# Optimization experiments

Hardware: AMD Instinct MI355X
Metric: run time of the kernel (lower is better)

The kernel has to match this reference:

```python
import jax, jax.numpy as jnp
import numpy as np

B, N, L = 16, 512, 512          # batch, compound atoms, protein words
DIM = 10                         # compound feature dim
DM, H, DK, DFF = 128, 8, 16, 512 # transformer dims
LG, LO = 3, 3                    # layer_gnn, layer_output
NFP, NW = 10000, 10000           # vocab sizes
NEG = -9e15                      # GAT mask sentinel (matches torch code)


def _layernorm(x, g, b, eps=1e-6):
    # annotated-transformer LayerNorm: unbiased std, eps added to std
    m = jnp.mean(x, -1, keepdims=True)
    s = jnp.std(x, -1, keepdims=True, ddof=1)
    return g * (x - m) / (s + eps) + b


def _pos_encoding(length, d_model):
    pos = np.arange(length)[:, None]
    div = np.exp(np.arange(0, d_model, 2) * (-np.log(10000.0) / d_model))
    pe = np.zeros((length, d_model), np.float32)
    pe[:, 0::2] = np.sin(pos * div)
    pe[:, 1::2] = np.cos(pos * div)
    return jnp.asarray(pe)


def setup_inputs():
    ks = iter(jax.random.split(jax.random.key(0), 64))
    def nrm(shape, scale):
        return jax.random.normal(next(ks), shape, jnp.float32) * scale
    return dict(
        fingerprints=jax.random.randint(next(ks), (B, N), 0, NFP, jnp.int32),
        fp_mask=jnp.ones((B, N), jnp.float32),
        adjacency=jax.random.randint(next(ks), (B, N, N), 0, 2, jnp.int32),
        words=jax.random.randint(next(ks), (B, L), 0, NW, jnp.int32),
        words_mask=jnp.ones((B, L), jnp.float32),
        emb_fp=nrm((NFP, DIM), 0.1),
        emb_word=nrm((NW, DM), 0.1),
        Wg=nrm((LG, DIM, DIM), 0.3), bg=jnp.zeros((LG, DIM), jnp.float32),
        attn_a=nrm((LG, 2 * DIM), 0.3),
        Wq=nrm((DM, DM), 0.09), bq=jnp.zeros((DM,), jnp.float32),
        Wk=nrm((DM, DM), 0.09), bk=jnp.zeros((DM,), jnp.float32),
        Wv=nrm((DM, DM), 0.09), bv=jnp.zeros((DM,), jnp.float32),
        Wo=nrm((DM, DM), 0.09), bo=jnp.zeros((DM,), jnp.float32),
        ln1_g=jnp.ones((DM,), jnp.float32), ln1_b=jnp.zeros((DM,), jnp.float32),
        ln2_g=jnp.ones((DM,), jnp.float32), ln2_b=jnp.zeros((DM,), jnp.float32),
        lnf_g=jnp.ones((DM,), jnp.float32), lnf_b=jnp.zeros((DM,), jnp.float32),
        W1=nrm((DM, DFF), 0.09), b1=jnp.zeros((DFF,), jnp.float32),
        W2=nrm((DFF, DM), 0.045), b2=jnp.zeros((DM,), jnp.float32),
        Wtout=nrm((DM, DIM), 0.09), btout=jnp.zeros((DIM,), jnp.float32),
        Watt=nrm((DIM, DIM), 0.3), batt=jnp.zeros((DIM,), jnp.float32),
        Wout=nrm((LO, 2 * DIM, 2 * DIM), 0.2), bout=jnp.zeros((LO, 2 * DIM), jnp.float32),
        Wint=nrm((2 * DIM, 2), 0.2), bint=jnp.zeros((2,), jnp.float32),
    )


def _forward(fingerprints, fp_mask, adjacency, words, words_mask,
             emb_fp, emb_word, Wg, bg, attn_a,
             Wq, bq, Wk, bk, Wv, bv, Wo, bo,
             ln1_g, ln1_b, ln2_g, ln2_b, lnf_g, lnf_b,
             W1, b1, W2, b2, Wtout, btout,
             Watt, batt, Wout, bout, Wint, bint):
    # ---- GAT over compound graph (dropout disabled = eval/deterministic) ----
    xs = emb_fp[fingerprints]                     # [B,N,DIM]
    mask = fp_mask[:, :, None]                    # [B,N,1]
    adj = adjacency > 0
    for i in range(LG):
        h = jax.nn.relu(xs @ Wg[i] + bg[i]) * mask
        # e[b,i,j] = leaky_relu(a1.h_i + a2.h_j)  == leaky_relu([h_i||h_j] @ a)
        s1 = h @ attn_a[i, :DIM]                  # [B,N]
        s2 = h @ attn_a[i, DIM:]                  # [B,N]
        e = jax.nn.leaky_relu(s1[:, :, None] + s2[:, None, :])  # [B,N,N]
        att = jax.nn.softmax(jnp.where(adj, e, NEG), axis=2)
        xs = xs + att @ h
    compound = jnp.mean(xs * mask, axis=1, keepdims=True)       # [B,1,DIM]

    # ---- transformer encoder, 1 layer, annotated-transformer (pre-norm) ----
    x = emb_word[words] * jnp.sqrt(jnp.float32(DM)) + _pos_encoding(L, DM)
    m4 = words_mask[:, None, None, :] > 0         # [B,1,1,L]
    xn = _layernorm(x, ln1_g, ln1_b)
    heads = lambda t: t.reshape(B, L, H, DK).transpose(0, 2, 1, 3)
    q, k, v = heads(xn @ Wq + bq), heads(xn @ Wk + bk), heads(xn @ Wv + bv)
    scores = jnp.einsum('bhqd,bhkd->bhqk', q, k) / jnp.sqrt(jnp.float32(DK))
    p = jax.nn.softmax(jnp.where(m4, scores, -1e9), axis=-1)
    attn = jnp.einsum('bhqk,bhkd->bhqd', p, v).transpose(0, 2, 1, 3).reshape(B, L, DM)
    x = x + (attn @ Wo + bo)
    xn = _layernorm(x, ln2_g, ln2_b)
    x = x + (jax.nn.relu(xn @ W1 + b1) @ W2 + b2)
    x = _layernorm(x, lnf_g, lnf_b)
    word_vectors = jax.nn.relu(x) @ Wtout + btout  # [B,L,DIM]

    # ---- tanh cross-attention (attention_cnn) ----
    hc = jax.nn.relu(compound @ Watt + batt)       # [B,1,DIM]
    hp = jax.nn.relu(word_vectors @ Watt + batt)   # [B,L,DIM]
    w = jnp.tanh(jnp.einsum('bxd,bld->bxl', hc, hp))  # [B,1,L]
    protein = jnp.mean(w.transpose(0, 2, 1) * hp, axis=1, keepdims=True)  # [B,1,DIM]

    cat = jnp.concatenate([compound, protein], axis=2)  # [B,1,2*DIM]
    for j in range(LO):
        cat = jax.nn.relu(cat @ Wout[j] + bout[j])
    return jnp.squeeze(cat @ Wint + bint, axis=1)        # [B,2]


def reference(fingerprints, fp_mask, adjacency, words, words_mask,
              emb_fp, emb_word, Wg, bg, attn_a,
              Wq, bq, Wk, bk, Wv, bv, Wo, bo,
              ln1_g, ln1_b, ln2_g, ln2_b, lnf_g, lnf_b,
              W1, b1, W2, b2, Wtout, btout,
              Watt, batt, Wout, bout, Wint, bint):
    return _forward(fingerprints, fp_mask, adjacency, words, words_mask,
                    emb_fp, emb_word, Wg, bg, attn_a,
                    Wq, bq, Wk, bk, Wv, bv, Wo, bo,
                    ln1_g, ln1_b, ln2_g, ln2_b, lnf_g, lnf_b,
                    W1, b1, W2, b2, Wtout, btout,
                    Watt, batt, Wout, bout, Wint, bint)
```

## Files before the change

kernel.cpp:

```cpp
#include <hip/hip_runtime.h>
#include <hip/hip_bf16.h>
#include <math.h>

#define B 16
#define N 512
#define L 512
#define DIM 10
#define DM 128
#define H 8
#define DK 16
#define DFF 512
#define LG 3
#define LO 3
#define NEGV -9.0e15f
#define RF 16
#define AQR 64

__device__ __forceinline__ float wave_reduce_sum(float v) {
    #pragma unroll
    for (int o = 32; o > 0; o >>= 1) v += __shfl_down(v, o, 64);
    return v;
}

__device__ __forceinline__ float quad_sum(float x) {
    int y1 = __builtin_amdgcn_mov_dpp(__float_as_int(x), 0xB1, 0xF, 0xF, true);
    float s = x + __int_as_float(y1);
    int y2 = __builtin_amdgcn_mov_dpp(__float_as_int(s), 0x4E, 0xF, 0xF, true);
    return s + __int_as_float(y2);
}


__global__ void k_embed_fp(const int* __restrict__ fing, const float* __restrict__ emb_fp,
                           float* __restrict__ xs) {
    int idx = blockIdx.x * blockDim.x + threadIdx.x;
    if (idx >= B * N * DIM) return;
    int d = idx % DIM;
    int bn = idx / DIM;
    xs[idx] = emb_fp[fing[bn] * DIM + d];
}

__global__ void k_gnn_h(const float* __restrict__ xs, const float* __restrict__ fp_mask,
                        const float* __restrict__ Wg, const float* __restrict__ bg,
                        const float* __restrict__ aatt,
                        float* __restrict__ h, float* __restrict__ s1, float* __restrict__ s2) {
    int bn = blockIdx.x * blockDim.x + threadIdx.x;
    if (bn >= B * N) return;
    float x[DIM];
    #pragma unroll
    for (int d = 0; d < DIM; d++) x[d] = xs[bn * DIM + d];
    float m = fp_mask[bn];
    float a1 = 0.f, a2 = 0.f;
    #pragma unroll
    for (int j = 0; j < DIM; j++) {
        float acc = bg[j];
        #pragma unroll
        for (int d = 0; d < DIM; d++) acc += x[d] * Wg[d * DIM + j];
        acc = fmaxf(acc, 0.f) * m;
        h[bn * DIM + j] = acc;
        a1 += acc * aatt[j];
        a2 += acc * aatt[DIM + j];
    }
    s1[bn] = a1;
    s2[bn] = a2;
}

__global__ void k_gnn_att(const float* __restrict__ h, const float* __restrict__ s1,
                          const float* __restrict__ s2, const int* __restrict__ adj,
                          float* __restrict__ xs) {
    int b  = blockIdx.x / (N / 16);
    int rg = blockIdx.x % (N / 16);
    int t = threadIdx.x;
    int g  = t >> 4;
    int ll = t & 15;
    int i = rg * 16 + g;

    __shared__ float h_s[N * DIM];
    __shared__ float s2_s[N];

    const float* hb = h + (long)b * N * DIM;
    for (int idx = t; idx < N * DIM; idx += 256) h_s[idx] = hb[idx];
    for (int j = t; j < N; j += 256) s2_s[j] = s2[b * N + j];
    __syncthreads();

    float s1v = s1[b * N + i];
    const int* adjrow = adj + ((long)b * N + i) * N;

    float e[32];
    #pragma unroll
    for (int c = 0; c < 32; c++) {
        int j = c * 16 + ll;
        float xsc = s1v + s2_s[j];
        xsc = xsc > 0.f ? xsc : 0.01f * xsc;
        e[c] = (adjrow[j] > 0) ? xsc : NEGV;
    }
    float m = e[0];
    #pragma unroll
    for (int c = 1; c < 32; c++) m = fmaxf(m, e[c]);
    #pragma unroll
    for (int off = 1; off < 16; off <<= 1) m = fmaxf(m, __shfl_xor(m, off, 64));

    float sum = 0.f;
    float a[DIM];
    #pragma unroll
    for (int d = 0; d < DIM; d++) a[d] = 0.f;
    #pragma unroll
    for (int c = 0; c < 32; c++) {
        float p = expf(e[c] - m);
        sum += p;
        int j = c * 16 + ll;
        #pragma unroll
        for (int d = 0; d < DIM; d++) a[d] += p * h_s[j * DIM + d];
    }
    #pragma unroll
    for (int off = 1; off < 16; off <<= 1) {
        sum += __shfl_xor(sum, off, 64);
        #pragma unroll
        for (int d = 0; d < DIM; d++) a[d] += __shfl_xor(a[d], off, 64);
    }
    if (ll < DIM) {
        float av = a[0];
        if (ll == 1) av = a[1]; else if (ll == 2) av = a[2]; else if (ll == 3) av = a[3];
        else if (ll == 4) av = a[4]; else if (ll == 5) av = a[5]; else if (ll == 6) av = a[6];
        else if (ll == 7) av = a[7]; else if (ll == 8) av = a[8]; else if (ll == 9) av = a[9];
        xs[((long)b * N + i) * DIM + ll] += av / sum;
    }
}

__global__ void k_compound(const float* __restrict__ xs, const float* __restrict__ fp_mask,
                           const float* __restrict__ Watt, const float* __restrict__ batt,
                           float* __restrict__ compound, float* __restrict__ hc) {
    int b = blockIdx.x;
    int t = threadIdx.x;
    int wid = t >> 6, lane = t & 63;
    float lacc[DIM];
    #pragma unroll
    for (int d = 0; d < DIM; d++) lacc[d] = 0.f;
    for (int n = t; n < N; n += 256) {
        float m = fp_mask[b * N + n];
        #pragma unroll
        for (int d = 0; d < DIM; d++) lacc[d] += xs[((long)b * N + n) * DIM + d] * m;
    }
    __shared__ float red[4][DIM];
    __shared__ float comp_s[DIM];
    #pragma unroll
    for (int d = 0; d < DIM; d++) lacc[d] = wave_reduce_sum(lacc[d]);
    if (lane == 0) {
        #pragma unroll
        for (int d = 0; d < DIM; d++) red[wid][d] = lacc[d];
    }
    __syncthreads();
    if (t < DIM) {
        float c = (red[0][t] + red[1][t] + red[2][t] + red[3][t]) / (float)N;
        compound[b * DIM + t] = c;
        comp_s[t] = c;
    }
    __syncthreads();
    if (t < DIM) {
        float acc = batt[t];
        #pragma unroll
        for (int e = 0; e < DIM; e++) acc += comp_s[e] * Watt[e * DIM + t];
        hc[b * DIM + t] = fmaxf(acc, 0.f);
    }
}


__global__ void k_pe(float* __restrict__ pe) {
    int idx = blockIdx.x * blockDim.x + threadIdx.x;
    if (idx >= L * DM) return;
    int d = idx % DM, l = idx / DM;
    int k = d >> 1;
    double div = exp((double)(2 * k) * (-log(10000.0) / (double)DM));
    double ang = (double)l * div;
    pe[idx] = (d & 1) ? (float)cos(ang) : (float)sin(ang);
}

__global__ void k_embed_word(const int* __restrict__ words, const float* __restrict__ emb,
                             const float* __restrict__ pe, float* __restrict__ x) {
    long idx = (long)blockIdx.x * blockDim.x + threadIdx.x;
    if (idx >= (long)B * L * DM) return;
    int d = idx % DM;
    long bl = idx / DM;
    int l = (int)(bl % L);
    x[idx] = emb[(long)words[bl] * DM + d] * sqrtf(128.0f) + pe[l * DM + d];
}

__global__ void k_layernorm(const float* __restrict__ x, const float* __restrict__ g,
                            const float* __restrict__ bb, float* __restrict__ out) {
    int row = blockIdx.x;
    int t = threadIdx.x;
    int wid = t >> 6, lane = t & 63;
    float v = x[(long)row * DM + t];
    float s = wave_reduce_sum(v);
    __shared__ float r2[2], r3[2];
    if (lane == 0) r2[wid] = s;
    __syncthreads();
    float mean = (r2[0] + r2[1]) / (float)DM;
    float dv = v - mean;
    float q = wave_reduce_sum(dv * dv);
    if (lane == 0) r3[wid] = q;
    __syncthreads();
    float sd = sqrtf((r3[0] + r3[1]) / (float)(DM - 1)) + 1e-6f;
    out[(long)row * DM + t] = g[t] * dv / sd + bb[t];
}

__global__ void k_qkv(const float* __restrict__ xn,
                      const float* __restrict__ Wq, const float* __restrict__ bq,
                      const float* __restrict__ Wk, const float* __restrict__ bk,
                      const float* __restrict__ Wv, const float* __restrict__ bv,
                      float* __restrict__ q, float* __restrict__ k, float* __restrict__ v) {
    long row0 = (long)blockIdx.x * RF;
    int t = threadIdx.x;
    __shared__ float xs_s[RF * DM];
    for (int i = t; i < RF * DM; i += 384) xs_s[i] = xn[row0 * DM + i];
    __syncthreads();
    int proj = t / DM;
    int j = t % DM;
    const float* W    = proj == 0 ? Wq : (proj == 1 ? Wk : Wv);
    const float* bias = proj == 0 ? bq : (proj == 1 ? bk : bv);
    float* out        = proj == 0 ? q  : (proj == 1 ? k  : v);
    float acc[RF];
    #pragma unroll
    for (int r = 0; r < RF; r++) acc[r] = bias[j];
    for (int d = 0; d < DM; d++) {
        float w = W[d * DM + j];
        #pragma unroll
        for (int r = 0; r < RF; r++) acc[r] += xs_s[r * DM + d] * w;
    }
    #pragma unroll
    for (int r = 0; r < RF; r++) {
        long row = row0 + r;
        int b = (int)(row / L), l = (int)(row % L);
        out[(((long)b * H + j / DK) * L + l) * DK + (j % DK)] = acc[r];
    }
}

__global__ void __launch_bounds__(256, 4)
k_attn(const float* __restrict__ q, const float* __restrict__ k,
       const float* __restrict__ v, const float* __restrict__ wmask,
       float* __restrict__ attnout) {
    int blk = blockIdx.x;
    int qc = blk % (L / AQR);
    int bh = blk / (L / AQR);
    int b = bh / H, hh = bh % H;
    int t = threadIdx.x;
    int sl = t & 3;
    int r = t >> 2;
    int l = qc * AQR + r;

    __shared__ float4 k_s[L * 4];
    __shared__ float wm_s[L];
    const float4* kb4 = (const float4*)(k + (long)bh * L * DK);
    for (int i = t; i < L * 4; i += 256) k_s[i] = kb4[i];
    for (int j = t; j < L; j += 256) wm_s[j] = (wmask[b * L + j] > 0.f) ? 0.f : -1e9f;
    __syncthreads();

    float4 qr = ((const float4*)(q + ((long)bh * L + l) * DK))[sl];
    qr.x *= 0.25f; qr.y *= 0.25f; qr.z *= 0.25f; qr.w *= 0.25f;

    const float4* vb4 = (const float4*)(v + (long)bh * L * DK);

    float m = -1e30f, ssum = 0.f;
    float4 acc = make_float4(0.f, 0.f, 0.f, 0.f);

    for (int c = 0; c < L / 8; c++) {
        int j0 = c * 8;
        float s8[8];
        #pragma unroll
        for (int jj = 0; jj < 8; jj++) {
            float4 kk = k_s[(j0 + jj) * 4 + sl];
            float part = qr.x * kk.x + qr.y * kk.y + qr.z * kk.z + qr.w * kk.w;
            s8[jj] = quad_sum(part);
        }
        const float4* mp = (const float4*)&wm_s[j0];
        float4 ma = mp[0], mb = mp[1];
        s8[0] += ma.x; s8[1] += ma.y; s8[2] += ma.z; s8[3] += ma.w;
        s8[4] += mb.x; s8[5] += mb.y; s8[6] += mb.z; s8[7] += mb.w;

        float cm = fmaxf(fmaxf(fmaxf(s8[0], s8[1]), fmaxf(s8[2], s8[3])),
                         fmaxf(fmaxf(s8[4], s8[5]), fmaxf(s8[6], s8[7])));
        float mn = fmaxf(m, cm);
        float scale = __expf(m - mn);
        ssum *= scale;
        acc.x *= scale; acc.y *= scale; acc.z *= scale; acc.w *= scale;
        m = mn;
        #pragma unroll
        for (int jj = 0; jj < 8; jj++) {
            float p = __expf(s8[jj] - m);
            ssum += p;
            float4 vv = vb4[(j0 + jj) * 4 + sl];
            acc.x += p * vv.x; acc.y += p * vv.y; acc.z += p * vv.z; acc.w += p * vv.w;
        }
    }

    float inv = 1.f / ssum;
    float4* outp = (float4*)(attnout + ((long)b * L + l) * DM + hh * DK);
    outp[sl] = make_float4(acc.x * inv, acc.y * inv, acc.z * inv, acc.w * inv);
}

__global__ void k_oproj(const float* __restrict__ attnout, const float* __restrict__ Wo,
                        const float* __restrict__ bo, float* __restrict__ x) {
    long row0 = (long)blockIdx.x * RF;
    int t = threadIdx.x;
    __shared__ float a_s[RF * DM];
    for (int i = t; i < RF * DM; i += 128) a_s[i] = attnout[row0 * DM + i];
    __syncthreads();
    float acc[RF];
    #pragma unroll
    for (int r = 0; r < RF; r++) acc[r] = bo[t];
    for (int d = 0; d < DM; d++) {
        float w = Wo[d * DM + t];
        #pragma unroll
        for (int r = 0; r < RF; r++) acc[r] += a_s[r * DM + d] * w;
    }
    #pragma unroll
    for (int r = 0; r < RF; r++) x[(row0 + r) * DM + t] += acc[r];
}

__global__ void k_ffn(const float* __restrict__ xn, const float* __restrict__ W1,
                      const float* __restrict__ b1, const float* __restrict__ W2,
                      const float* __restrict__ b2, float* __restrict__ x) {
    long row0 = (long)blockIdx.x * RF;
    int t = threadIdx.x;
    __shared__ float xs_s[RF * DM];
    __shared__ float h_s[RF * DFF];
    for (int i = t; i < RF * DM; i += 512) xs_s[i] = xn[row0 * DM + i];
    __syncthreads();
    {
        float acc[RF];
        #pragma unroll
        for (int r = 0; r < RF; r++) acc[r] = b1[t];
        for (int d = 0; d < DM; d++) {
            float w = W1[d * DFF + t];
            #pragma unroll
            for (int r = 0; r < RF; r++) acc[r] += xs_s[r * DM + d] * w;
        }
        #pragma unroll
        for (int r = 0; r < RF; r++) h_s[r * DFF + t] = fmaxf(acc[r], 0.f);
    }
    __syncthreads();
    int col = t & 127, rq = t >> 7;
    float acc2[4];
    #pragma unroll
    for (int rr = 0; rr < 4; rr++) acc2[rr] = b2[col];
    for (int f = 0; f < DFF; f++) {
        float w = W2[f * DM + col];
        #pragma unroll
        for (int rr = 0; rr < 4; rr++) acc2[rr] += h_s[(rq * 4 + rr) * DFF + f] * w;
    }
    #pragma unroll
    for (int rr = 0; rr < 4; rr++) x[(row0 + rq * 4 + rr) * DM + col] += acc2[rr];
}

__global__ void k_lnf_hp(const float* __restrict__ x, const float* __restrict__ g,
                         const float* __restrict__ bb, const float* __restrict__ Wtout,
                         const float* __restrict__ btout, const float* __restrict__ Watt,
                         const float* __restrict__ batt, float* __restrict__ hp) {
    int row = blockIdx.x;
    int t = threadIdx.x;
    int wid = t >> 6, lane = t & 63;
    float v = x[(long)row * DM + t];
    float s = wave_reduce_sum(v);
    __shared__ float r2[2], r3[2];
    if (lane == 0) r2[wid] = s;
    __syncthreads();
    float mean = (r2[0] + r2[1]) / (float)DM;
    float dv = v - mean;
    float qq = wave_reduce_sum(dv * dv);
    if (lane == 0) r3[wid] = qq;
    __syncthreads();
    float sd = sqrtf((r3[0] + r3[1]) / (float)(DM - 1)) + 1e-6f;
    float xnv = g[t] * dv / sd + bb[t];
    __shared__ float rrelu[DM];
    rrelu[t] = fmaxf(xnv, 0.f);
    __syncthreads();
    __shared__ float wv_s[DIM];
    if (t < DIM) {
        float acc = btout[t];
        for (int d = 0; d < DM; d++) acc += rrelu[d] * Wtout[d * DIM + t];
        wv_s[t] = acc;
    }
    __syncthreads();
    if (t < DIM) {
        float acc = batt[t];
        #pragma unroll
        for (int e = 0; e < DIM; e++) acc += wv_s[e] * Watt[e * DIM + t];
        hp[(long)row * DIM + t] = fmaxf(acc, 0.f);
    }
}

__global__ void k_final(const float* __restrict__ hp, const float* __restrict__ hc,
                        const float* __restrict__ compound, const float* __restrict__ Wout,
                        const float* __restrict__ bout, const float* __restrict__ Wint,
                        const float* __restrict__ bint, float* __restrict__ out) {
    int b = blockIdx.x;
    int t = threadIdx.x;
    int wid = t >> 6, lane = t & 63;

    __shared__ float wout_s[LO * 2 * DIM * 2 * DIM];
    __shared__ float bout_s[LO * 2 * DIM];
    __shared__ float wint_s[2 * DIM * 2];
    __shared__ float bint_s[2];
    __shared__ float hc_s[DIM];
    __shared__ float red[4][DIM];
    __shared__ float cat_s[2 * DIM];
    __shared__ float tmp_s[2 * DIM];

    for (int i = t; i < LO * 2 * DIM * 2 * DIM; i += 256) wout_s[i] = Wout[i];
    for (int i = t; i < LO * 2 * DIM; i += 256) bout_s[i] = bout[i];
    for (int i = t; i < 2 * DIM * 2; i += 256) wint_s[i] = Wint[i];
    if (t < 2) bint_s[t] = bint[t];
    if (t < DIM) hc_s[t] = hc[b * DIM + t];
    __syncthreads();

    float lacc[DIM];
    #pragma unroll
    for (int e = 0; e < DIM; e++) lacc[e] = 0.f;
    for (int l = t; l < L; l += 256) {
        const float* hpl = hp + ((long)b * L + l) * DIM;
        float hv[DIM];
        float dot = 0.f;
        #pragma unroll
        for (int e = 0; e < DIM; e++) { hv[e] = hpl[e]; dot += hc_s[e] * hv[e]; }
        float w = tanhf(dot);
        #pragma unroll
        for (int e = 0; e < DIM; e++) lacc[e] += w * hv[e];
    }
    #pragma unroll
    for (int e = 0; e < DIM; e++) lacc[e] = wave_reduce_sum(lacc[e]);
    if (lane == 0) {
        #pragma unroll
        for (int e = 0; e < DIM; e++) red[wid][e] = lacc[e];
    }
    __syncthreads();
    if (t < DIM) {
        cat_s[t] = compound[b * DIM + t];
        cat_s[DIM + t] = (red[0][t] + red[1][t] + red[2][t] + red[3][t]) / (float)L;
    }
    __syncthreads();

    for (int j = 0; j < LO; j++) {
        float acc = 0.f;
        if (t < 2 * DIM) {
            acc = bout_s[j * 2 * DIM + t];
            #pragma unroll
            for (int e = 0; e < 2 * DIM; e++)
                acc += cat_s[e] * wout_s[j * 2 * DIM * 2 * DIM + e * 2 * DIM + t];
            acc = fmaxf(acc, 0.f);
            tmp_s[t] = acc;
        }
        __syncthreads();
        if (t < 2 * DIM) cat_s[t] = tmp_s[t];
        __syncthreads();
    }
    if (t < 2) {
        float o = bint_s[t];
        #pragma unroll
        for (int e = 0; e < 2 * DIM; e++) o += cat_s[e] * wint_s[e * 2 + t];
        out[b * 2 + t] = o;
    }
}

extern "C" void kernel_launch(void* const* d_in, const int* in_sizes, int n_in,
                              void* d_out, int out_size, void* d_ws, size_t ws_size,
                              hipStream_t stream) {
    (void)in_sizes; (void)n_in; (void)out_size; (void)ws_size;
    const int*   fingerprints = (const int*)d_in[0];
    const float* fp_mask      = (const float*)d_in[1];
    const int*   adjacency    = (const int*)d_in[2];
    const int*   words        = (const int*)d_in[3];
    const float* words_mask   = (const float*)d_in[4];
    const float* emb_fp       = (const float*)d_in[5];
    const float* emb_word     = (const float*)d_in[6];
    const float* Wg   = (const float*)d_in[7];
    const float* bg   = (const float*)d_in[8];
    const float* attn_a = (const float*)d_in[9];
    const float* Wq = (const float*)d_in[10];
    const float* bq = (const float*)d_in[11];
    const float* Wk = (const float*)d_in[12];
    const float* bk = (const float*)d_in[13];
    const float* Wv = (const float*)d_in[14];
    const float* bv = (const float*)d_in[15];
    const float* Wo = (const float*)d_in[16];
    const float* bo = (const float*)d_in[17];
    const float* ln1_g = (const float*)d_in[18];
    const float* ln1_b = (const float*)d_in[19];
    const float* ln2_g = (const float*)d_in[20];
    const float* ln2_b = (const float*)d_in[21];
    const float* lnf_g = (const float*)d_in[22];
    const float* lnf_b = (const float*)d_in[23];
    const float* W1 = (const float*)d_in[24];
    const float* b1 = (const float*)d_in[25];
    const float* W2 = (const float*)d_in[26];
    const float* b2 = (const float*)d_in[27];
    const float* Wtout = (const float*)d_in[28];
    const float* btout = (const float*)d_in[29];
    const float* Watt  = (const float*)d_in[30];
    const float* batt  = (const float*)d_in[31];
    const float* Wout  = (const float*)d_in[32];
    const float* bout  = (const float*)d_in[33];
    const float* Wint  = (const float*)d_in[34];
    const float* bint  = (const float*)d_in[35];
    float* out = (float*)d_out;

    float* w = (float*)d_ws;
    float* xs = w;        w += B * N * DIM;
    float* h  = w;        w += B * N * DIM;
    float* s1 = w;        w += B * N;
    float* s2 = w;        w += B * N;
    float* compound = w;  w += B * DIM;
    float* hc = w;        w += B * DIM;
    float* pe = w;        w += L * DM;
    float* x  = w;        w += (long)B * L * DM;
    float* xn = w;        w += (long)B * L * DM;
    float* qb = w;        w += (long)B * H * L * DK;
    float* kb = w;        w += (long)B * H * L * DK;
    float* vb = w;        w += (long)B * H * L * DK;
    float* attnout = w;   w += (long)B * L * DM;
    float* hp = w;        w += (long)B * L * DIM;

    k_embed_fp<<<(B * N * DIM + 255) / 256, 256, 0, stream>>>(fingerprints, emb_fp, xs);
    for (int i = 0; i < LG; i++) {
        k_gnn_h<<<(B * N + 255) / 256, 256, 0, stream>>>(
            xs, fp_mask, Wg + i * DIM * DIM, bg + i * DIM, attn_a + i * 2 * DIM, h, s1, s2);
        k_gnn_att<<<B * (N / 16), 256, 0, stream>>>(h, s1, s2, adjacency, xs);
    }
    k_compound<<<B, 256, 0, stream>>>(xs, fp_mask, Watt, batt, compound, hc);

    k_pe<<<(L * DM + 255) / 256, 256, 0, stream>>>(pe);
    k_embed_word<<<(B * L * DM + 255) / 256, 256, 0, stream>>>(words, emb_word, pe, x);
    k_layernorm<<<B * L, DM, 0, stream>>>(x, ln1_g, ln1_b, xn);
    k_qkv<<<B * L / RF, 3 * DM, 0, stream>>>(xn, Wq, bq, Wk, bk, Wv, bv, qb, kb, vb);
    k_attn<<<B * H * (L / AQR), 256, 0, stream>>>(qb, kb, vb, words_mask, attnout);
    k_oproj<<<B * L / RF, DM, 0, stream>>>(attnout, Wo, bo, x);
    k_layernorm<<<B * L, DM, 0, stream>>>(x, ln2_g, ln2_b, xn);
    k_ffn<<<B * L / RF, DFF, 0, stream>>>(xn, W1, b1, W2, b2, x);
    k_lnf_hp<<<B * L, DM, 0, stream>>>(x, lnf_g, lnf_b, Wtout, btout, Watt, batt, hp);
    k_final<<<B, 256, 0, stream>>>(hp, hc, compound, Wout, bout, Wint, bint, out);
}
```

Before: 255.2 us.

## Fuse embedding with LayerNorm and LN2, FFN, final LN and head into one kernel

Merges word embedding and the first LayerNorm into one kernel. It also folds the second LayerNorm, the FFN, the final LayerNorm and the small output projections into a single per-16-row kernel, so the residual stream no longer round-trips through global memory between these stages. The QKV, O-projection and FFN matmul inner loops are unrolled by four with float4 shared-memory reads to cut LDS instruction count. The fused FFN kernel uses more shared memory per block (about 50KB), which may lower occupancy.

```diff
diff --git a/kernel.cpp b/kernel.cpp
--- a/kernel.cpp
+++ b/kernel.cpp
@@ -29,6 +29,12 @@
     return s + __int_as_float(y2);
 }
 
+__device__ __forceinline__ float half_reduce_sum(float v) {
+    #pragma unroll
+    for (int o = 16; o > 0; o >>= 1) v += __shfl_xor(v, o, 64);
+    return v;
+}
+
 
 __global__ void k_embed_fp(const int* __restrict__ fing, const float* __restrict__ emb_fp,
                            float* __restrict__ xs) {
@@ -174,22 +180,16 @@
     pe[idx] = (d & 1) ? (float)cos(ang) : (float)sin(ang);
 }
 
-__global__ void k_embed_word(const int* __restrict__ words, const float* __restrict__ emb,
-                             const float* __restrict__ pe, float* __restrict__ x) {
-    long idx = (long)blockIdx.x * blockDim.x + threadIdx.x;
-    if (idx >= (long)B * L * DM) return;
-    int d = idx % DM;
-    long bl = idx / DM;
-    int l = (int)(bl % L);
-    x[idx] = emb[(long)words[bl] * DM + d] * sqrtf(128.0f) + pe[l * DM + d];
-}
-
-__global__ void k_layernorm(const float* __restrict__ x, const float* __restrict__ g,
-                            const float* __restrict__ bb, float* __restrict__ out) {
+__global__ void k_embed_ln(const int* __restrict__ words, const float* __restrict__ emb,
+                           const float* __restrict__ pe, const float* __restrict__ g,
+                           const float* __restrict__ bb,
+                           float* __restrict__ x, float* __restrict__ xn) {
     int row = blockIdx.x;
     int t = threadIdx.x;
     int wid = t >> 6, lane = t & 63;
-    float v = x[(long)row * DM + t];
+    int l = row % L;
+    float v = emb[(long)words[row] * DM + t] * sqrtf(128.0f) + pe[l * DM + t];
+    x[(long)row * DM + t] = v;
     float s = wave_reduce_sum(v);
     __shared__ float r2[2], r3[2];
     if (lane == 0) r2[wid] = s;
@@ -200,7 +200,7 @@
     if (lane == 0) r3[wid] = q;
     __syncthreads();
     float sd = sqrtf((r3[0] + r3[1]) / (float)(DM - 1)) + 1e-6f;
-    out[(long)row * DM + t] = g[t] * dv / sd + bb[t];
+    xn[(long)row * DM + t] = g[t] * dv / sd + bb[t];
 }
 
 __global__ void k_qkv(const float* __restrict__ xn,
@@ -221,10 +221,16 @@
     float acc[RF];
     #pragma unroll
     for (int r = 0; r < RF; r++) acc[r] = bias[j];
-    for (int d = 0; d < DM; d++) {
-        float w = W[d * DM + j];
-        #pragma unroll
-        for (int r = 0; r < RF; r++) acc[r] += xs_s[r * DM + d] * w;
+    for (int d4 = 0; d4 < DM / 4; d4++) {
+        float w0 = W[(4 * d4 + 0) * DM + j];
+        float w1 = W[(4 * d4 + 1) * DM + j];
+        float w2 = W[(4 * d4 + 2) * DM + j];
+        float w3 = W[(4 * d4 + 3) * DM + j];
+        #pragma unroll
+        for (int r = 0; r < RF; r++) {
+            float4 xv = ((const float4*)&xs_s[r * DM])[d4];
+            acc[r] += xv.x * w0 + xv.y * w1 + xv.z * w2 + xv.w * w3;
+        }
     }
     #pragma unroll
     for (int r = 0; r < RF; r++) {
@@ -307,84 +313,142 @@
     float acc[RF];
     #pragma unroll
     for (int r = 0; r < RF; r++) acc[r] = bo[t];
-    for (int d = 0; d < DM; d++) {
-        float w = Wo[d * DM + t];
-        #pragma unroll
-        for (int r = 0; r < RF; r++) acc[r] += a_s[r * DM + d] * w;
+    for (int d4 = 0; d4 < DM / 4; d4++) {
+        float w0 = Wo[(4 * d4 + 0) * DM + t];
+        float w1 = Wo[(4 * d4 + 1) * DM + t];
+        float w2 = Wo[(4 * d4 + 2) * DM + t];
+        float w3 = Wo[(4 * d4 + 3) * DM + t];
+        #pragma unroll
+        for (int r = 0; r < RF; r++) {
+            float4 av = ((const float4*)&a_s[r * DM])[d4];
+            acc[r] += av.x * w0 + av.y * w1 + av.z * w2 + av.w * w3;
+        }
     }
     #pragma unroll
     for (int r = 0; r < RF; r++) x[(row0 + r) * DM + t] += acc[r];
 }
 
-__global__ void k_ffn(const float* __restrict__ xn, const float* __restrict__ W1,
-                      const float* __restrict__ b1, const float* __restrict__ W2,
-                      const float* __restrict__ b2, float* __restrict__ x) {
+__global__ void k_ffn_fused(const float* __restrict__ x,
+                            const float* __restrict__ ln2_g, const float* __restrict__ ln2_b,
+                            const float* __restrict__ W1, const float* __restrict__ b1,
+                            const float* __restrict__ W2, const float* __restrict__ b2,
+                            const float* __restrict__ lnf_g, const float* __restrict__ lnf_b,
+                            const float* __restrict__ Wtout, const float* __restrict__ btout,
+                            const float* __restrict__ Watt, const float* __restrict__ batt,
+                            float* __restrict__ hp) {
     long row0 = (long)blockIdx.x * RF;
     int t = threadIdx.x;
-    __shared__ float xs_s[RF * DM];
-    __shared__ float h_s[RF * DFF];
-    for (int i = t; i < RF * DM; i += 512) xs_s[i] = xn[row0 * DM + i];
-    __syncthreads();
+
+    __shared__ float x_s[RF][DM];
+    __shared__ float xn_s[RF][DM];
+    __shared__ float h_s[RF][DFF];
+    __shared__ float r_s[RF][DM + 4];
+    __shared__ float wt_s[DM * DIM];
+    __shared__ float wa_s[DIM * DIM];
+    __shared__ float bt_s[DIM], ba_s[DIM];
+    __shared__ float wv_s[RF][DIM];
+
+    {
+        float4 xv = ((const float4*)(x + row0 * DM))[t];
+        ((float4*)&x_s[0][0])[t] = xv;
+        for (int i = t; i < DM * DIM; i += 512) wt_s[i] = Wtout[i];
+        for (int i = t; i < DIM * DIM; i += 512) wa_s[i] = Watt[i];
+        if (t < DIM) { bt_s[t] = btout[t]; ba_s[t] = batt[t]; }
+    }
+    __syncthreads();
+
+    {
+        int row = t >> 5, c = t & 31;
+        float4 v = ((const float4*)&x_s[row][0])[c];
+        float s = half_reduce_sum(v.x + v.y + v.z + v.w);
+        float mean = s / (float)DM;
+        float4 dv = make_float4(v.x - mean, v.y - mean, v.z - mean, v.w - mean);
+        float q = half_reduce_sum(dv.x * dv.x + dv.y * dv.y + dv.z * dv.z + dv.w * dv.w);
+        float sd = sqrtf(q / (float)(DM - 1)) + 1e-6f;
+        const float4 g4 = ((const float4*)ln2_g)[c];
+        const float4 b4 = ((const float4*)ln2_b)[c];
+        ((float4*)&xn_s[row][0])[c] = make_float4(
+            g4.x * dv.x / sd + b4.x, g4.y * dv.y / sd + b4.y,
+            g4.z * dv.z / sd + b4.z, g4.w * dv.w / sd + b4.w);
+    }
+    __syncthreads();
+
     {
         float acc[RF];
         #pragma unroll
         for (int r = 0; r < RF; r++) acc[r] = b1[t];
-        for (int d = 0; d < DM; d++) {
-            float w = W1[d * DFF + t];
+        for (int d4 = 0; d4 < DM / 4; d4++) {
+            float w0 = W1[(4 * d4 + 0) * DFF + t];
+            float w1 = W1[(4 * d4 + 1) * DFF + t];
+            float w2 = W1[(4 * d4 + 2) * DFF + t];
+            float w3 = W1[(4 * d4 + 3) * DFF + t];
             #pragma unroll
-            for (int r = 0; r < RF; r++) acc[r] += xs_s[r * DM + d] * w;
-        }
-        #pragma unroll
-        for (int r = 0; r < RF; r++) h_s[r * DFF + t] = fmaxf(acc[r], 0.f);
-    }
-    __syncthreads();
-    int col = t & 127, rq = t >> 7;
-    float acc2[4];
-    #pragma unroll
-    for (int rr = 0; rr < 4; rr++) acc2[rr] = b2[col];
-    for (int f = 0; f < DFF; f++) {
-        float w = W2[f * DM + col];
-        #pragma unroll
-        for (int rr = 0; rr < 4; rr++) acc2[rr] += h_s[(rq * 4 + rr) * DFF + f] * w;
-    }
-    #pragma unroll
-    for (int rr = 0; rr < 4; rr++) x[(row0 + rq * 4 + rr) * DM + col] += acc2[rr];
-}
-
-__global__ void k_lnf_hp(const float* __restrict__ x, const float* __restrict__ g,
-                         const float* __restrict__ bb, const float* __restrict__ Wtout,
-                         const float* __restrict__ btout, const float* __restrict__ Watt,
-                         const float* __restrict__ batt, float* __restrict__ hp) {
-    int row = blockIdx.x;
-    int t = threadIdx.x;
-    int wid = t >> 6, lane = t & 63;
-    float v = x[(long)row * DM + t];
-    float s = wave_reduce_sum(v);
-    __shared__ float r2[2], r3[2];
-    if (lane == 0) r2[wid] = s;
-    __syncthreads();
-    float mean = (r2[0] + r2[1]) / (float)DM;
-    float dv = v - mean;
-    float qq = wave_reduce_sum(dv * dv);
-    if (lane == 0) r3[wid] = qq;
-    __syncthreads();
-    float sd = sqrtf((r3[0] + r3[1]) / (float)(DM - 1)) + 1e-6f;
-    float xnv = g[t] * dv / sd + bb[t];
-    __shared__ float rrelu[DM];
-    rrelu[t] = fmaxf(xnv, 0.f);
-    __syncthreads();
-    __shared__ float wv_s[DIM];
-    if (t < DIM) {
-        float acc = btout[t];
-        for (int d = 0; d < DM; d++) acc += rrelu[d] * Wtout[d * DIM + t];
-        wv_s[t] = acc;
-    }
-    __syncthreads();
-    if (t < DIM) {
-        float acc = batt[t];
-        #pragma unroll
-        for (int e = 0; e < DIM; e++) acc += wv_s[e] * Watt[e * DIM + t];
-        hp[(long)row * DIM + t] = fmaxf(acc, 0.f);
+            for (int r = 0; r < RF; r++) {
+                float4 xv = ((const float4*)&xn_s[r][0])[d4];
+                acc[r] += xv.x * w0 + xv.y * w1 + xv.z * w2 + xv.w * w3;
+            }
+        }
+        #pragma unroll
+        for (int r = 0; r < RF; r++) h_s[r][t] = fmaxf(acc[r], 0.f);
+    }
+    __syncthreads();
+
+    {
+        int col = t & 127, rq = t >> 7;
+        float acc2[4];
+        #pragma unroll
+        for (int rr = 0; rr < 4; rr++) acc2[rr] = b2[col];
+        for (int f4 = 0; f4 < DFF / 4; f4++) {
+            float w0 = W2[(4 * f4 + 0) * DM + col];
+            float w1 = W2[(4 * f4 + 1) * DM + col];
+            float w2 = W2[(4 * f4 + 2) * DM + col];
+            float w3 = W2[(4 * f4 + 3) * DM + col];
+            #pragma unroll
+            for (int rr = 0; rr < 4; rr++) {
+                float4 hv = ((const float4*)&h_s[rq * 4 + rr][0])[f4];
+                acc2[rr] += hv.x * w0 + hv.y * w1 + hv.z * w2 + hv.w * w3;
+            }
+        }
+        __syncthreads();
+        #pragma unroll
+        for (int rr = 0; rr < 4; rr++) {
+            int row = rq * 4 + rr;
+            xn_s[row][col] = x_s[row][col] + acc2[rr];
+        }
+    }
+    __syncthreads();
+
+    {
+        int row = t >> 5, c = t & 31;
+        float4 v = ((const float4*)&xn_s[row][0])[c];
+        float s = half_reduce_sum(v.x + v.y + v.z + v.w);
+        float mean = s / (float)DM;
+        float4 dv = make_float4(v.x - mean, v.y - mean, v.z - mean, v.w - mean);
+        float q = half_reduce_sum(dv.x * dv.x + dv.y * dv.y + dv.z * dv.z + dv.w * dv.w);
+        float sd = sqrtf(q / (float)(DM - 1)) + 1e-6f;
+        const float4 g4 = ((const float4*)lnf_g)[c];
+        const float4 b4 = ((const float4*)lnf_b)[c];
+        r_s[row][4 * c + 0] = fmaxf(g4.x * dv.x / sd + b4.x, 0.f);
+        r_s[row][4 * c + 1] = fmaxf(g4.y * dv.y / sd + b4.y, 0.f);
+        r_s[row][4 * c + 2] = fmaxf(g4.z * dv.z / sd + b4.z, 0.f);
+        r_s[row][4 * c + 3] = fmaxf(g4.w * dv.w / sd + b4.w, 0.f);
+    }
+    __syncthreads();
+
+    if (t < RF * DIM) {
+        int row = t / DIM, o = t % DIM;
+        float acc = bt_s[o];
+        for (int d = 0; d < DM; d++) acc += r_s[row][d] * wt_s[d * DIM + o];
+        wv_s[row][o] = acc;
+    }
+    __syncthreads();
+
+    if (t < RF * DIM) {
+        int row = t / DIM, o = t % DIM;
+        float acc = ba_s[o];
+        #pragma unroll
+        for (int e = 0; e < DIM; e++) acc += wv_s[row][e] * wa_s[e * DIM + o];
+        hp[(row0 + row) * DIM + o] = fmaxf(acc, 0.f);
     }
 }
 
@@ -527,13 +591,11 @@
     k_compound<<<B, 256, 0, stream>>>(xs, fp_mask, Watt, batt, compound, hc);
 
     k_pe<<<(L * DM + 255) / 256, 256, 0, stream>>>(pe);
-    k_embed_word<<<(B * L * DM + 255) / 256, 256, 0, stream>>>(words, emb_word, pe, x);
-    k_layernorm<<<B * L, DM, 0, stream>>>(x, ln1_g, ln1_b, xn);
+    k_embed_ln<<<B * L, DM, 0, stream>>>(words, emb_word, pe, ln1_g, ln1_b, x, xn);
     k_qkv<<<B * L / RF, 3 * DM, 0, stream>>>(xn, Wq, bq, Wk, bk, Wv, bv, qb, kb, vb);
     k_attn<<<B * H * (L / AQR), 256, 0, stream>>>(qb, kb, vb, words_mask, attnout);
     k_oproj<<<B * L / RF, DM, 0, stream>>>(attnout, Wo, bo, x);
-    k_layernorm<<<B * L, DM, 0, stream>>>(x, ln2_g, ln2_b, xn);
-    k_ffn<<<B * L / RF, DFF, 0, stream>>>(xn, W1, b1, W2, b2, x);
-    k_lnf_hp<<<B * L, DM, 0, stream>>>(x, lnf_g, lnf_b, Wtout, btout, Watt, batt, hp);
+    k_ffn_fused<<<B * L / RF, DFF, 0, stream>>>(x, ln2_g, ln2_b, W1, b1, W2, b2,
+                                                lnf_g, lnf_b, Wtout, btout, Watt, batt, hp);
     k_final<<<B, 256, 0, stream>>>(hp, hc, compound, Wout, bout, Wint, bint, out);
 }
```

New measurement: 246.3 us (median of 2 runs). 3.5% less time.
